# Kernel tuning notes

Measured on AMD Instinct MI355X. Metric: run time of the kernel, lower is better.

Reference implementation:

```python
import jax, jax.numpy as jnp
import numpy as np

N_BINS = 15


def setup_inputs() -> dict:
    key = jax.random.key(0)
    k1, k2 = jax.random.split(key)
    N, C = 50000, 1000
    logits = jax.random.normal(k1, (N, C), dtype=jnp.float32)
    labels = jax.random.randint(k2, (N,), 0, C, dtype=jnp.int32)
    return {"logits": logits, "labels": labels, "num_classes": C}


def reference(logits, labels, num_classes):
    """Per-class ECE (SCE) + per-class top-1 accuracy.

    Faithful to the torch double loop over classes x bins, vectorized as a
    single scatter-add (segment_sum) over (class, bin) segments.
    """
    n_bins = N_BINS
    N = logits.shape[0]
    probs = jax.nn.softmax(logits, axis=1)           # [N, C]
    choices = jnp.argmax(probs, axis=1)              # [N]

    # bin k covers (k/n_bins, (k+1)/n_bins]; conf == 0 falls in no bin -> id -1
    bounds = jnp.linspace(0.0, 1.0, n_bins + 1)
    bin_id = jnp.searchsorted(bounds, probs, side='left') - 1  # [N, C]

    class_idx = jnp.arange(num_classes)
    # flatten (class, bin) into segment ids; invalid bins dumped into extra seg
    seg = jnp.where(bin_id >= 0,
                    class_idx[None, :] * n_bins + bin_id,
                    num_classes * n_bins).reshape(-1)
    conf_flat = probs.reshape(-1)
    lab_match = (labels[:, None] == class_idx[None, :]).astype(probs.dtype).reshape(-1)

    n_seg = num_classes * n_bins + 1
    sum_conf = jax.ops.segment_sum(conf_flat, seg, num_segments=n_seg)[:-1].reshape(num_classes, n_bins)
    sum_lab = jax.ops.segment_sum(lab_match, seg, num_segments=n_seg)[:-1].reshape(num_classes, n_bins)

    # sum_b |avg_conf_b - acc_b| * prop_b == sum_b |sum_conf_b - sum_lab_b| / N
    # (bins with zero count contribute exactly 0, matching the torch guard)
    per_class_sce = jnp.sum(jnp.abs(sum_conf - sum_lab), axis=1) / N

    correct = jax.ops.segment_sum((choices == labels).astype(jnp.float32), labels,
                                  num_segments=num_classes)
    total = jax.ops.segment_sum(jnp.ones(N, jnp.float32), labels,
                                num_segments=num_classes)
    classes_acc = correct / total
    return per_class_sce, classes_acc
```

## Files before the change

kernel.cpp:

```cpp
#include <hip/hip_runtime.h>
#include <math.h>

#define NBINS 15
#define BIN0_HI (1.0f / 15.0f)

__global__ void zero_ws(float* __restrict__ ws, int n) {
    int i = blockIdx.x * blockDim.x + threadIdx.x;
    const int stride = gridDim.x * blockDim.x;
    for (; i < n; i += stride) ws[i] = 0.0f;
}

__global__ __launch_bounds__(256) void row_stats(
    const float* __restrict__ logits, const int* __restrict__ labels,
    float2* __restrict__ rowstats, float* __restrict__ g_lab,
    float* __restrict__ g_cor, float* __restrict__ g_tot, int N, int C) {
    const int lane = threadIdx.x & 63;
    const int gw = blockIdx.x * (blockDim.x >> 6) + (threadIdx.x >> 6);
    const int nw = gridDim.x * (blockDim.x >> 6);
    const int nf4 = C >> 2;

    for (int row = gw; row < N; row += nw) {
        const float4* rp = (const float4*)(logits + (size_t)row * C);
        float4 x[4];
#pragma unroll
        for (int k = 0; k < 4; ++k) {
            const int idx = k * 64 + lane;
            if (idx < nf4) x[k] = rp[idx];
            else x[k] = make_float4(-INFINITY, -INFINITY, -INFINITY, -INFINITY);
        }

        float bv = -INFINITY;
        int bi = 0x7fffffff;
#pragma unroll
        for (int k = 0; k < 4; ++k) {
            const int c0 = (k * 64 + lane) * 4;
            const float xv[4] = {x[k].x, x[k].y, x[k].z, x[k].w};
#pragma unroll
            for (int j = 0; j < 4; ++j) {
                const float v = xv[j];
                if (v > bv || (v == bv && (c0 + j) < bi)) { bv = v; bi = c0 + j; }
            }
        }
#pragma unroll
        for (int off = 32; off > 0; off >>= 1) {
            const float ov = __shfl_xor(bv, off);
            const int oi = __shfl_xor(bi, off);
            if (ov > bv || (ov == bv && oi < bi)) { bv = ov; bi = oi; }
        }
        const float m = bv;

        float s = 0.0f;
#pragma unroll
        for (int k = 0; k < 4; ++k) {
            x[k].x = __expf(x[k].x - m);
            x[k].y = __expf(x[k].y - m);
            x[k].z = __expf(x[k].z - m);
            x[k].w = __expf(x[k].w - m);
            s += (x[k].x + x[k].y) + (x[k].z + x[k].w);
        }
#pragma unroll
        for (int off = 32; off > 0; off >>= 1) s += __shfl_xor(s, off);
        const float inv = 1.0f / s;

        const int label = labels[row];

        const int fi = label >> 2;
        if ((fi & 63) == lane) {
            const int k = fi >> 6, j = label & 3;
            const float4 v = (k == 0) ? x[0] : (k == 1) ? x[1] : (k == 2) ? x[2] : x[3];
            const float e = (j == 0) ? v.x : (j == 1) ? v.y : (j == 2) ? v.z : v.w;
            const float p = e * inv;
            if (p > 0.0f) {
                int b;
                if (p <= BIN0_HI) b = 0;
                else { b = (int)ceilf(p * 15.0f) - 1; b = b < 1 ? 1 : (b > 14 ? 14 : b); }
                atomicAdd(&g_lab[label * NBINS + b], 1.0f);
            }
        }
        if (lane == 0) {
            rowstats[row] = make_float2(m, inv);
            atomicAdd(&g_tot[label], 1.0f);
            if (bi == label) atomicAdd(&g_cor[label], 1.0f);
        }
    }
}

__global__ __launch_bounds__(256) void col_bin(
    const float* __restrict__ logits, const float2* __restrict__ rowstats,
    float* __restrict__ partial, float* __restrict__ g_rare,
    int N, int C, int R) {
    const int t = threadIdx.x;
    const int c0 = t * 4;
    if (c0 >= C) return;
    const int r0 = blockIdx.x * R;
    const int r1 = min(N, r0 + R);

    float a0 = 0.f, a1 = 0.f, a2 = 0.f, a3 = 0.f;
    for (int r = r0; r < r1; ++r) {
        const float4 x = *(const float4*)(logits + (size_t)r * C + c0);
        const float2 st = rowstats[r];
        const float p0 = __expf(x.x - st.x) * st.y;
        const float p1 = __expf(x.y - st.x) * st.y;
        const float p2 = __expf(x.z - st.x) * st.y;
        const float p3 = __expf(x.w - st.x) * st.y;
        const bool s0 = p0 > BIN0_HI, s1 = p1 > BIN0_HI, s2 = p2 > BIN0_HI, s3 = p3 > BIN0_HI;
        a0 += s0 ? 0.f : p0;
        a1 += s1 ? 0.f : p1;
        a2 += s2 ? 0.f : p2;
        a3 += s3 ? 0.f : p3;
        if (__any(s0 | s1 | s2 | s3)) {
            const float pv[4] = {p0, p1, p2, p3};
            const bool sv[4] = {s0, s1, s2, s3};
#pragma unroll
            for (int j = 0; j < 4; ++j) {
                if (sv[j]) {
                    int b = (int)ceilf(pv[j] * 15.0f) - 1;
                    b = b < 1 ? 1 : (b > 14 ? 14 : b);
                    atomicAdd(&g_rare[(c0 + j) * NBINS + b], pv[j]);
                }
            }
        }
    }
    float4 out;
    out.x = a0; out.y = a1; out.z = a2; out.w = a3;
    *(float4*)(partial + (size_t)blockIdx.x * C + c0) = out;
}

__global__ __launch_bounds__(256) void finalize_k(
    const float* __restrict__ partial, const float* __restrict__ g_rare,
    const float* __restrict__ g_lab, const float* __restrict__ g_cor,
    const float* __restrict__ g_tot, float* __restrict__ out,
    int N, int C, int NC) {
    const int lane = threadIdx.x & 63;
    const int c = blockIdx.x * (blockDim.x >> 6) + (threadIdx.x >> 6);
    if (c >= C) return;
    float s = 0.0f;
    for (int i = lane; i < NC; i += 64) s += partial[(size_t)i * C + c];
#pragma unroll
    for (int off = 32; off > 0; off >>= 1) s += __shfl_xor(s, off);
    if (lane == 0) {
        float tsum = fabsf(s + g_rare[c * NBINS] - g_lab[c * NBINS]);
#pragma unroll
        for (int b = 1; b < NBINS; ++b)
            tsum += fabsf(g_rare[c * NBINS + b] - g_lab[c * NBINS + b]);
        out[c] = tsum / (float)N;
        out[C + c] = g_cor[c] / g_tot[c];
    }
}

extern "C" void kernel_launch(void* const* d_in, const int* in_sizes, int n_in,
                              void* d_out, int out_size, void* d_ws, size_t ws_size,
                              hipStream_t stream) {
    const float* logits = (const float*)d_in[0];
    const int* labels = (const int*)d_in[1];
    const int N = in_sizes[1];
    const int C = in_sizes[0] / in_sizes[1];

    float* f = (float*)d_ws;
    float2* rowstats = (float2*)f;
    float* g_lab = f + (size_t)2 * N;
    float* g_rare = g_lab + (size_t)C * NBINS;
    float* g_cor = g_rare + (size_t)C * NBINS;
    float* g_tot = g_cor + C;
    float* partial = g_tot + C;

    const size_t fixed = (size_t)2 * N + (size_t)2 * C * NBINS + (size_t)2 * C;
    long avail = (long)(ws_size / 4) - (long)fixed;
    long ncmax = avail > 0 ? avail / C : 1;
    int NC = (int)(ncmax < 1 ? 1 : (ncmax > 2048 ? 2048 : ncmax));
    if (NC > N) NC = N;
    const int R = (N + NC - 1) / NC;
    NC = (N + R - 1) / R;

    zero_ws<<<64, 256, 0, stream>>>(g_lab, 2 * C * NBINS + 2 * C);

    row_stats<<<2048, 256, 0, stream>>>(logits, labels, rowstats, g_lab,
                                        g_cor, g_tot, N, C);

    col_bin<<<NC, 256, 0, stream>>>(logits, rowstats, partial, g_rare, N, C, R);

    finalize_k<<<(C + 3) / 4, 256, 0, stream>>>(partial, g_rare, g_lab, g_cor,
                                                g_tot, (float*)d_out, N, C, NC);
}
```

Baseline: 394.2 us.

## Fuse row-stats and column-binning passes into a single logits read

Result: no change. 387.2 us (-1.8%).

```diff
diff --git a/kernel.cpp b/kernel.cpp
--- a/kernel.cpp
+++ b/kernel.cpp
@@ -10,14 +10,21 @@
     for (; i < n; i += stride) ws[i] = 0.0f;
 }
 
-__global__ __launch_bounds__(256) void row_stats(
+__global__ __launch_bounds__(512) void fused_pass(
     const float* __restrict__ logits, const int* __restrict__ labels,
-    float2* __restrict__ rowstats, float* __restrict__ g_lab,
-    float* __restrict__ g_cor, float* __restrict__ g_tot, int N, int C) {
-    const int lane = threadIdx.x & 63;
-    const int gw = blockIdx.x * (blockDim.x >> 6) + (threadIdx.x >> 6);
+    float* __restrict__ partial, float* __restrict__ g_rare,
+    float* __restrict__ g_lab, float* __restrict__ g_cor,
+    float* __restrict__ g_tot, int N, int C) {
+    extern __shared__ float s_colsum[];
+    const int tid = threadIdx.x;
+    const int lane = tid & 63;
+    const int gw = blockIdx.x * (blockDim.x >> 6) + (tid >> 6);
     const int nw = gridDim.x * (blockDim.x >> 6);
     const int nf4 = C >> 2;
+
+    float4 acc[4];
+#pragma unroll
+    for (int k = 0; k < 4; ++k) acc[k] = make_float4(0.f, 0.f, 0.f, 0.f);
 
     for (int row = gw; row < N; row += nw) {
         const float4* rp = (const float4*)(logits + (size_t)row * C);
@@ -78,52 +85,52 @@
             }
         }
         if (lane == 0) {
-            rowstats[row] = make_float2(m, inv);
             atomicAdd(&g_tot[label], 1.0f);
             if (bi == label) atomicAdd(&g_cor[label], 1.0f);
         }
-    }
-}
 
-__global__ __launch_bounds__(256) void col_bin(
-    const float* __restrict__ logits, const float2* __restrict__ rowstats,
-    float* __restrict__ partial, float* __restrict__ g_rare,
-    int N, int C, int R) {
-    const int t = threadIdx.x;
-    const int c0 = t * 4;
-    if (c0 >= C) return;
-    const int r0 = blockIdx.x * R;
-    const int r1 = min(N, r0 + R);
-
-    float a0 = 0.f, a1 = 0.f, a2 = 0.f, a3 = 0.f;
-    for (int r = r0; r < r1; ++r) {
-        const float4 x = *(const float4*)(logits + (size_t)r * C + c0);
-        const float2 st = rowstats[r];
-        const float p0 = __expf(x.x - st.x) * st.y;
-        const float p1 = __expf(x.y - st.x) * st.y;
-        const float p2 = __expf(x.z - st.x) * st.y;
-        const float p3 = __expf(x.w - st.x) * st.y;
-        const bool s0 = p0 > BIN0_HI, s1 = p1 > BIN0_HI, s2 = p2 > BIN0_HI, s3 = p3 > BIN0_HI;
-        a0 += s0 ? 0.f : p0;
-        a1 += s1 ? 0.f : p1;
-        a2 += s2 ? 0.f : p2;
-        a3 += s3 ? 0.f : p3;
-        if (__any(s0 | s1 | s2 | s3)) {
-            const float pv[4] = {p0, p1, p2, p3};
-            const bool sv[4] = {s0, s1, s2, s3};
 #pragma unroll
-            for (int j = 0; j < 4; ++j) {
-                if (sv[j]) {
-                    int b = (int)ceilf(pv[j] * 15.0f) - 1;
-                    b = b < 1 ? 1 : (b > 14 ? 14 : b);
-                    atomicAdd(&g_rare[(c0 + j) * NBINS + b], pv[j]);
+        for (int k = 0; k < 4; ++k) {
+            const float p0 = x[k].x * inv, p1 = x[k].y * inv;
+            const float p2 = x[k].z * inv, p3 = x[k].w * inv;
+            const bool r0 = p0 > BIN0_HI, r1 = p1 > BIN0_HI;
+            const bool r2 = p2 > BIN0_HI, r3 = p3 > BIN0_HI;
+            acc[k].x += r0 ? 0.f : p0;
+            acc[k].y += r1 ? 0.f : p1;
+            acc[k].z += r2 ? 0.f : p2;
+            acc[k].w += r3 ? 0.f : p3;
+            if (__any(r0 | r1 | r2 | r3)) {
+                const int c0 = (k * 64 + lane) * 4;
+                const float pv[4] = {p0, p1, p2, p3};
+                const bool rv[4] = {r0, r1, r2, r3};
+#pragma unroll
+                for (int j = 0; j < 4; ++j) {
+                    if (rv[j]) {
+                        int b = (int)ceilf(pv[j] * 15.0f) - 1;
+                        b = b < 1 ? 1 : (b > 14 ? 14 : b);
+                        atomicAdd(&g_rare[(c0 + j) * NBINS + b], pv[j]);
+                    }
                 }
             }
         }
     }
-    float4 out;
-    out.x = a0; out.y = a1; out.z = a2; out.w = a3;
-    *(float4*)(partial + (size_t)blockIdx.x * C + c0) = out;
+
+    for (int i = tid; i < C; i += blockDim.x) s_colsum[i] = 0.0f;
+    __syncthreads();
+#pragma unroll
+    for (int k = 0; k < 4; ++k) {
+        const int idx = k * 64 + lane;
+        if (idx < nf4) {
+            const int c0 = idx * 4;
+            atomicAdd(&s_colsum[c0 + 0], acc[k].x);
+            atomicAdd(&s_colsum[c0 + 1], acc[k].y);
+            atomicAdd(&s_colsum[c0 + 2], acc[k].z);
+            atomicAdd(&s_colsum[c0 + 3], acc[k].w);
+        }
+    }
+    __syncthreads();
+    for (int i = tid; i < C; i += blockDim.x)
+        partial[(size_t)blockIdx.x * C + i] = s_colsum[i];
 }
 
 __global__ __launch_bounds__(256) void finalize_k(
@@ -157,28 +164,22 @@
     const int C = in_sizes[0] / in_sizes[1];
 
     float* f = (float*)d_ws;
-    float2* rowstats = (float2*)f;
-    float* g_lab = f + (size_t)2 * N;
+    float* g_lab = f;
     float* g_rare = g_lab + (size_t)C * NBINS;
     float* g_cor = g_rare + (size_t)C * NBINS;
     float* g_tot = g_cor + C;
     float* partial = g_tot + C;
 
-    const size_t fixed = (size_t)2 * N + (size_t)2 * C * NBINS + (size_t)2 * C;
+    const size_t fixed = (size_t)2 * C * NBINS + (size_t)2 * C;
     long avail = (long)(ws_size / 4) - (long)fixed;
-    long ncmax = avail > 0 ? avail / C : 1;
-    int NC = (int)(ncmax < 1 ? 1 : (ncmax > 2048 ? 2048 : ncmax));
-    if (NC > N) NC = N;
-    const int R = (N + NC - 1) / NC;
-    NC = (N + R - 1) / R;
+    long gmax = avail > 0 ? avail / C : 64;
+    int GRID = (int)(gmax < 64 ? 64 : (gmax > 1024 ? 1024 : gmax));
 
-    zero_ws<<<64, 256, 0, stream>>>(g_lab, 2 * C * NBINS + 2 * C);
+    zero_ws<<<64, 256, 0, stream>>>(f, 2 * C * NBINS + 2 * C);
 
-    row_stats<<<2048, 256, 0, stream>>>(logits, labels, rowstats, g_lab,
-                                        g_cor, g_tot, N, C);
-
-    col_bin<<<NC, 256, 0, stream>>>(logits, rowstats, partial, g_rare, N, C, R);
+    fused_pass<<<GRID, 512, (size_t)C * sizeof(float), stream>>>(
+        logits, labels, partial, g_rare, g_lab, g_cor, g_tot, N, C);
 
     finalize_k<<<(C + 3) / 4, 256, 0, stream>>>(partial, g_rare, g_lab, g_cor,
-                                                g_tot, (float*)d_out, N, C, NC);
+                                                g_tot, (float*)d_out, N, C, GRID);
 }
```
